# Optimization experiments

Hardware: AMD Instinct MI355X
Metric: run time of the kernel (lower is better)

The kernel has to match this reference:

```python
import jax, jax.numpy as jnp
import numpy as np

RATIO = 4   # compression ratio (group size)
H = 6       # index heads
D = 64      # index head dim = max(8, 768//6//2)
TOPK = 8    # index_topk
EPS = 1e-6  # rms_norm eps


def rms_norm(x):
    return x * jax.lax.rsqrt(jnp.mean(jnp.square(x), axis=-1, keepdims=True) + EPS)


def setup_inputs() -> dict:
    key = jax.random.key(0)
    k1, k2, k3, k4, k5 = jax.random.split(key, 5)
    B, T, E = 4, 4096, 768
    s = 0.02
    return {
        "x": jax.random.normal(k1, (B, T, E), jnp.float32),
        "wq": jax.random.normal(k2, (E, H * D), jnp.float32) * s,
        "wk": jax.random.normal(k3, (E, H * D), jnp.float32) * s,
        "wg": jax.random.normal(k4, (E, H * D), jnp.float32) * s,
        "ape": jax.random.normal(k5, (RATIO, H, D), jnp.float32) * s,
    }


def reference(x, wq, wk, wg, ape):
    B, T, E = x.shape
    G = -(-T // RATIO)          # ceil(T / ratio)
    pad = G * RATIO - T

    # --- compress keys: gated pooling over ratio-groups ---
    k = (x @ wk).reshape(B, T, H, D)
    gate = (x @ wg).reshape(B, T, H, D)
    if pad:
        k = jnp.pad(k, ((0, 0), (0, pad), (0, 0), (0, 0)))
        gate = jnp.pad(gate, ((0, 0), (0, pad), (0, 0), (0, 0)), constant_values=-jnp.inf)
    k = k.reshape(B, G, RATIO, H, D)
    gate = gate.reshape(B, G, RATIO, H, D) + ape[None, None]
    w = jax.nn.softmax(gate.astype(jnp.float32), axis=2).astype(k.dtype)
    keys = rms_norm(jnp.sum(k * w, axis=2))           # [B,G,H,D]
    group_ends = jnp.minimum(jnp.arange(RATIO - 1, G * RATIO, RATIO), T - 1)  # [G]

    # --- query-key scores ---
    q = rms_norm((x @ wq).reshape(B, T, H, D))
    scores = jnp.einsum('bthd,bghd->bhtg', q, keys) * (D ** -0.5)
    scores = jnp.mean(scores, axis=1)                 # [B,T,G]

    # --- causal mask over group ends, then top-k selection ---
    causal = group_ends[None, None, :] <= jnp.arange(T)[None, :, None]  # [1,T,G]
    scores = jnp.where(causal, scores, -jnp.inf)
    topk = min(TOPK, G)
    _, sel = jax.lax.top_k(scores, topk)              # [B,T,topk]

    # scatter selected indices into boolean mask
    bi = jnp.arange(B)[:, None, None]
    ti = jnp.arange(T)[None, :, None]
    mask = jnp.zeros((B, T, G), dtype=bool).at[bi, ti, sel].set(True)
    return (mask & causal, group_ends)
```

## Files before the change

kernel.cpp:

```cpp
#include <hip/hip_runtime.h>
#include <hip/hip_bf16.h>
#include <math.h>

#define B_    4
#define T_    4096
#define E_    768
#define H_    6
#define D_    64
#define HD_   384
#define G_    1024
#define RATIO_ 4
#define TOPK_ 8
#define MT_   (B_*T_)
#define NS_   1152

typedef __attribute__((ext_vector_type(8))) short short8;
typedef __attribute__((ext_vector_type(4))) float f32x4;
typedef __hip_bfloat16 bf16;

#define GLD16(g, l) __builtin_amdgcn_global_load_lds( \
    (const __attribute__((address_space(1))) void*)(g), \
    (__attribute__((address_space(3))) void*)(l), 16, 0, 0)

static __device__ __forceinline__ unsigned short f2bf(float f) {
  bf16 h = __float2bfloat16(f);
  return __builtin_bit_cast(unsigned short, h);
}

__global__ __launch_bounds__(256) void cvt_x_kernel(
    const float* __restrict__ in, bf16* __restrict__ out)
{
  size_t i = (size_t)blockIdx.x * 256 + threadIdx.x;
  const float4* p = reinterpret_cast<const float4*>(in) + i * 2;
  float4 v0 = p[0], v1 = p[1];
  float f[8] = {v0.x, v0.y, v0.z, v0.w, v1.x, v1.y, v1.z, v1.w};
  union { unsigned short u[8]; short8 v; } r;
#pragma unroll
  for (int k = 0; k < 8; ++k) r.u[k] = f2bf(f[k]);
  *reinterpret_cast<short8*>(out + i * 8) = r.v;
}

__global__ __launch_bounds__(256) void cvt_w_t(
    const float* __restrict__ wq, const float* __restrict__ wk,
    const float* __restrict__ wg, bf16* __restrict__ outbase)
{
  const int z = blockIdx.z;
  const float* src = z == 0 ? wq : (z == 1 ? wk : wg);
  __shared__ float t[32][33];
  int r = threadIdx.x >> 5, c = threadIdx.x & 31;
  int k0 = blockIdx.x * 32, n0 = blockIdx.y * 32;
#pragma unroll
  for (int i = 0; i < 4; ++i)
    t[r + i * 8][c] = src[(size_t)(k0 + r + i * 8) * HD_ + n0 + c];
  __syncthreads();
#pragma unroll
  for (int i = 0; i < 4; ++i) {
    int cc = n0 + r + i * 8;
    int ro = (z == 0) ? cc : 384 + ((cc >> 4) << 5) + ((z - 1) << 4) + (cc & 15);
    outbase[(size_t)ro * E_ + k0 + c] = __float2bfloat16(t[c][r + i * 8]);
  }
}

__global__ __launch_bounds__(256, 3) void gemm_qkg_mfma(
    const bf16* __restrict__ X, const bf16* __restrict__ Ws,
    const float* __restrict__ ape, bf16* __restrict__ Q,
    bf16* __restrict__ keys)
{
  __shared__ bf16 lds[3][4096];
  const int tid = threadIdx.x;
  const int lane = tid & 63, wv = tid >> 6;
  const int ll = lane & 15, lh = lane >> 4;
  const int m0 = blockIdx.x * 128, n0 = blockIdx.y * 128;
  const int srow = tid >> 2;
  const int scol = (((tid & 3) ^ ((tid >> 3) & 3)) << 3);
  const bf16* pB0 = Ws + (size_t)(n0 + srow) * E_ + scol;
  const bf16* pB1 = Ws + (size_t)(n0 + 64 + srow) * E_ + scol;
  const bf16* pA0 = X + (size_t)(m0 + wv * 32 + ll) * E_ + lh * 8;
  const bf16* pA1 = pA0 + (size_t)16 * E_;

#define STAGE(b, k0) do { \
    char* base_ = (char*)&lds[b][0] + tid * 16; \
    GLD16(pB0 + (k0), base_); \
    GLD16(pB1 + (k0), base_ + 4096); \
  } while (0)

  f32x4 acc[2][8];
#pragma unroll
  for (int m = 0; m < 2; ++m)
#pragma unroll
    for (int n = 0; n < 8; ++n) acc[m][n] = (f32x4){0.f, 0.f, 0.f, 0.f};
  const int asw = (lh ^ ((ll >> 1) & 3)) << 3;

  short8 curA0 = *reinterpret_cast<const short8*>(pA0);
  short8 curA1 = *reinterpret_cast<const short8*>(pA1);
  STAGE(0, 0);
  STAGE(1, 32);
  short8 nxtA0 = curA0, nxtA1 = curA1;

#pragma unroll
  for (int k = 0; k < 24; ++k) {
    const int k0 = k * 32;
    if (k < 23) {
      nxtA0 = *reinterpret_cast<const short8*>(pA0 + k0 + 32);
      nxtA1 = *reinterpret_cast<const short8*>(pA1 + k0 + 32);
    }
    if (k < 22) STAGE((k + 2) % 3, k0 + 64);
    if (k < 22)       asm volatile("s_waitcnt vmcnt(6)" ::: "memory");
    else if (k == 22) asm volatile("s_waitcnt vmcnt(4)" ::: "memory");
    else              asm volatile("s_waitcnt vmcnt(0)" ::: "memory");
    __builtin_amdgcn_s_barrier();
    __builtin_amdgcn_sched_barrier(0);
    const bf16* Lb = &lds[k % 3][0];
    short8 b[8];
#pragma unroll
    for (int n = 0; n < 8; ++n)
      b[n] = *reinterpret_cast<const short8*>(&Lb[(n * 16 + ll) * 32 + asw]);
    asm volatile("s_waitcnt lgkmcnt(0)" ::: "memory");
    __builtin_amdgcn_sched_barrier(0);
    __builtin_amdgcn_s_barrier();
#pragma unroll
    for (int m = 0; m < 2; ++m) {
      short8 am = (m == 0) ? curA0 : curA1;
#pragma unroll
      for (int n = 0; n < 8; ++n)
        acc[m][n] = __builtin_amdgcn_mfma_f32_16x16x32_bf16(am, b[n], acc[m][n], 0, 0, 0);
    }
    curA0 = nxtA0; curA1 = nxtA1;
  }
#undef STAGE

  if (blockIdx.y < 3) {
#pragma unroll
    for (int m = 0; m < 2; ++m)
#pragma unroll
      for (int j = 0; j < 4; ++j) {
        int row = m0 + wv * 32 + m * 16 + lh * 4 + j;
#pragma unroll
        for (int h = 0; h < 2; ++h) {
          float ss = 0.f;
#pragma unroll
          for (int n = 4 * h; n < 4 * h + 4; ++n) ss += acc[m][n][j] * acc[m][n][j];
          ss += __shfl_xor(ss, 1, 64); ss += __shfl_xor(ss, 2, 64);
          ss += __shfl_xor(ss, 4, 64); ss += __shfl_xor(ss, 8, 64);
          float scl = rsqrtf(ss * (1.0f / D_) + 1e-6f);
#pragma unroll
          for (int n = 4 * h; n < 4 * h + 4; ++n)
            Q[(size_t)row * HD_ + n0 + n * 16 + ll] =
                __float2bfloat16(acc[m][n][j] * scl);
        }
      }
  } else {
    const int hcb = (n0 - 384) >> 1;
    float apev[4][4];
#pragma unroll
    for (int p = 0; p < 4; ++p) {
      int hc = hcb + p * 16 + ll;
#pragma unroll
      for (int j = 0; j < 4; ++j) apev[p][j] = ape[j * HD_ + hc];
    }
#pragma unroll
    for (int m = 0; m < 2; ++m) {
      float pooled[4];
#pragma unroll
      for (int p = 0; p < 4; ++p) {
        float g0 = acc[m][2 * p + 1][0] + apev[p][0];
        float g1 = acc[m][2 * p + 1][1] + apev[p][1];
        float g2 = acc[m][2 * p + 1][2] + apev[p][2];
        float g3 = acc[m][2 * p + 1][3] + apev[p][3];
        float mx = fmaxf(fmaxf(g0, g1), fmaxf(g2, g3));
        float e0 = expf(g0 - mx), e1 = expf(g1 - mx);
        float e2 = expf(g2 - mx), e3 = expf(g3 - mx);
        float inv = 1.0f / (e0 + e1 + e2 + e3);
        pooled[p] = (acc[m][2 * p][0] * e0 + acc[m][2 * p][1] * e1 +
                     acc[m][2 * p][2] * e2 + acc[m][2 * p][3] * e3) * inv;
      }
      float ss = pooled[0] * pooled[0] + pooled[1] * pooled[1] +
                 pooled[2] * pooled[2] + pooled[3] * pooled[3];
      ss += __shfl_xor(ss, 1, 64); ss += __shfl_xor(ss, 2, 64);
      ss += __shfl_xor(ss, 4, 64); ss += __shfl_xor(ss, 8, 64);
      float scl = rsqrtf(ss * (1.0f / D_) + 1e-6f);
      int prow = (m0 >> 2) + wv * 8 + m * 4 + lh;
#pragma unroll
      for (int p = 0; p < 4; ++p)
        keys[(size_t)prow * HD_ + hcb + p * 16 + ll] =
            __float2bfloat16(pooled[p] * scl);
    }
  }
}

__global__ __launch_bounds__(256, 4) void gemm_score_mfma(
    const bf16* __restrict__ Qall, const bf16* __restrict__ Kall,
    float* __restrict__ Call)
{
  const int m0 = blockIdx.x * 64, n0 = blockIdx.y * 128;
  if (4 * n0 >= m0 + 64) return;
  __shared__ bf16 lds[2][4096];
  const bf16* Qb = Qall + (size_t)blockIdx.z * T_ * HD_;
  const bf16* Kb = Kall + (size_t)blockIdx.z * G_ * HD_;
  float* C = Call + (size_t)blockIdx.z * T_ * G_;
  const int tid = threadIdx.x;
  const int lane = tid & 63, wv = tid >> 6;
  const int wm = wv >> 1, wn = wv & 1;
  const int ll = lane & 15, lh = lane >> 4;
  const int srow = tid >> 2;
  const int scol = (((tid & 3) ^ ((tid >> 3) & 3)) << 3);
  const bf16* pB0 = Kb + (size_t)(n0 + srow) * HD_ + scol;
  const bf16* pB1 = Kb + (size_t)(n0 + 64 + srow) * HD_ + scol;
  const bf16* pA0 = Qb + (size_t)(m0 + wm * 32 + ll) * HD_ + lh * 8;
  const bf16* pA1 = pA0 + (size_t)16 * HD_;

#define S_STAGE(b, k0) do { \
    char* base_ = (char*)&lds[b][0] + tid * 16; \
    GLD16(pB0 + (k0), base_); \
    GLD16(pB1 + (k0), base_ + 4096); \
  } while (0)

  f32x4 acc[2][4];
#pragma unroll
  for (int m = 0; m < 2; ++m)
#pragma unroll
    for (int n = 0; n < 4; ++n) acc[m][n] = (f32x4){0.f, 0.f, 0.f, 0.f};
  const int asw = (lh ^ ((ll >> 1) & 3)) << 3;

  S_STAGE(0, 0);
  __syncthreads();
  for (int k0 = 0; k0 < HD_; k0 += 32) {
    const int cur = (k0 >> 5) & 1;
    if (k0 + 32 < HD_) S_STAGE(cur ^ 1, k0 + 32);
    short8 a[2], b[4];
    a[0] = *reinterpret_cast<const short8*>(pA0 + k0);
    a[1] = *reinterpret_cast<const short8*>(pA1 + k0);
    const bf16* Lb = &lds[cur][0];
#pragma unroll
    for (int n = 0; n < 4; ++n)
      b[n] = *reinterpret_cast<const short8*>(&Lb[(wn * 64 + n * 16 + ll) * 32 + asw]);
#pragma unroll
    for (int m = 0; m < 2; ++m)
#pragma unroll
      for (int n = 0; n < 4; ++n)
        acc[m][n] = __builtin_amdgcn_mfma_f32_16x16x32_bf16(a[m], b[n], acc[m][n], 0, 0, 0);
    __syncthreads();
  }
#undef S_STAGE
  const float scale = 0.125f / 6.0f;
#pragma unroll
  for (int m = 0; m < 2; ++m)
#pragma unroll
    for (int j = 0; j < 4; ++j) {
      int row = m0 + wm * 32 + m * 16 + lh * 4 + j;
#pragma unroll
      for (int n = 0; n < 4; ++n)
        C[(size_t)row * G_ + n0 + wn * 64 + n * 16 + ll] = acc[m][n][j] * scale;
    }
}

__global__ __launch_bounds__(256) void topk_kernel(float* __restrict__ scores,
                                                   int* __restrict__ ends)
{
  if (blockIdx.x == 0) {
    int g = threadIdx.x;
#pragma unroll
    for (int c = 0; c < 4; ++c, g += 256) {
      int e = g * RATIO_ + RATIO_ - 1;
      ends[g] = (e < T_ - 1 ? e : T_ - 1);
    }
  }
  const int r = blockIdx.x * 4 + (threadIdx.x >> 6);
  const int lane = threadIdx.x & 63;
  const int t = r & (T_ - 1);
  const int gmax = (t + 1) >> 2;
  float* row = scores + (size_t)r * G_;
  const int base = lane << 4;
  const float4* p = reinterpret_cast<const float4*>(row + base);
  float4 xv[4];
#pragma unroll
  for (int c = 0; c < 4; ++c) {
    if (base + 4 * c < gmax) xv[c] = p[c];
    else xv[c] = make_float4(-INFINITY, -INFINITY, -INFINITY, -INFINITY);
  }
  float v[16] = {xv[0].x, xv[0].y, xv[0].z, xv[0].w,
                 xv[1].x, xv[1].y, xv[1].z, xv[1].w,
                 xv[2].x, xv[2].y, xv[2].z, xv[2].w,
                 xv[3].x, xv[3].y, xv[3].z, xv[3].w};
#pragma unroll
  for (int j = 0; j < 16; ++j)
    if (base + j >= gmax) v[j] = -INFINITY;
  float lv = v[0]; int li = 0;
#pragma unroll
  for (int j = 1; j < 16; ++j)
    if (v[j] > lv) { lv = v[j]; li = j; }
  unsigned sel = 0;
  const int nsel = gmax < TOPK_ ? gmax : TOPK_;
  for (int it = 0; it < nsel; ++it) {
    float bv = lv; int bi = base + li;
#pragma unroll
    for (int off = 1; off < 64; off <<= 1) {
      float ov = __shfl_xor(bv, off, 64);
      int oi = __shfl_xor(bi, off, 64);
      if (ov > bv || (ov == bv && oi < bi)) { bv = ov; bi = oi; }
    }
    if ((bi >> 4) == lane) {
      sel |= 1u << (bi & 15);
      v[bi & 15] = -INFINITY;
      lv = v[0]; li = 0;
#pragma unroll
      for (int j = 1; j < 16; ++j)
        if (v[j] > lv) { lv = v[j]; li = j; }
    }
  }
  int4* q = reinterpret_cast<int4*>(row + base);
#pragma unroll
  for (int c = 0; c < 4; ++c)
    q[c] = make_int4((sel >> (4 * c)) & 1, (sel >> (4 * c + 1)) & 1,
                     (sel >> (4 * c + 2)) & 1, (sel >> (4 * c + 3)) & 1);
}

extern "C" void kernel_launch(void* const* d_in, const int* in_sizes, int n_in,
                              void* d_out, int out_size, void* d_ws, size_t ws_size,
                              hipStream_t stream)
{
  const float* x   = (const float*)d_in[0];
  const float* wq  = (const float*)d_in[1];
  const float* wk  = (const float*)d_in[2];
  const float* wg  = (const float*)d_in[3];
  const float* ape = (const float*)d_in[4];

  bf16* Ws   = (bf16*)d_ws;
  bf16* qb   = Ws + (size_t)NS_ * E_;
  bf16* keys = qb + (size_t)MT_ * HD_;

  bf16* xb = (bf16*)d_out;

  cvt_x_kernel<<<dim3(MT_ * E_ / 8 / 256), dim3(256), 0, stream>>>(x, xb);
  cvt_w_t<<<dim3(E_ / 32, HD_ / 32, 3), dim3(256), 0, stream>>>(wq, wk, wg, Ws);

  gemm_qkg_mfma<<<dim3(MT_ / 128, NS_ / 128), dim3(256), 0, stream>>>(
      xb, Ws, ape, qb, keys);

  gemm_score_mfma<<<dim3(T_ / 64, G_ / 128, B_), dim3(256), 0, stream>>>(
      qb, keys, (float*)d_out);

  topk_kernel<<<dim3(MT_ / 4), dim3(256), 0, stream>>>(
      (float*)d_out, (int*)d_out + (size_t)B_ * T_ * G_);
}
```

Baseline: 124.1 us.

## Fuse score GEMM with register top-k using packed sortable keys

Replaces the separate score GEMM, which wrote a full fp32 score matrix, and the following top-k pass with one single-wave kernel per 16 query rows. Each wave streams key tiles through MFMA while holding its Q fragments in registers, packs each score with its index into a monotone unsigned key, and keeps a running top-8 through an insertion network. Lane results are merged with a shuffle-based bitonic merge, then the mask rows are zeroed and the selected entries set. This removes the round trip of the score matrix through memory, but it truncates score mantissa bits (so near-ties may resolve differently) and drops LDS reuse of K across waves.

```diff
diff --git a/kernel.cpp b/kernel.cpp
--- a/kernel.cpp
+++ b/kernel.cpp
@@ -26,6 +26,8 @@
   bf16 h = __float2bfloat16(f);
   return __builtin_bit_cast(unsigned short, h);
 }
+static __device__ __forceinline__ unsigned umax_(unsigned a, unsigned b) { return a > b ? a : b; }
+static __device__ __forceinline__ unsigned umin_(unsigned a, unsigned b) { return a > b ? b : a; }
 
 __global__ __launch_bounds__(256) void cvt_x_kernel(
     const float* __restrict__ in, bf16* __restrict__ out)
@@ -188,131 +190,126 @@
   }
 }
 
-__global__ __launch_bounds__(256, 4) void gemm_score_mfma(
+__global__ __launch_bounds__(64, 1) void score_topk_fused(
     const bf16* __restrict__ Qall, const bf16* __restrict__ Kall,
-    float* __restrict__ Call)
-{
-  const int m0 = blockIdx.x * 64, n0 = blockIdx.y * 128;
-  if (4 * n0 >= m0 + 64) return;
-  __shared__ bf16 lds[2][4096];
-  const bf16* Qb = Qall + (size_t)blockIdx.z * T_ * HD_;
-  const bf16* Kb = Kall + (size_t)blockIdx.z * G_ * HD_;
-  float* C = Call + (size_t)blockIdx.z * T_ * G_;
-  const int tid = threadIdx.x;
-  const int lane = tid & 63, wv = tid >> 6;
-  const int wm = wv >> 1, wn = wv & 1;
+    int* __restrict__ mask, int* __restrict__ ends)
+{
+  const int W = blockIdx.x;
+  const int lane = threadIdx.x;
   const int ll = lane & 15, lh = lane >> 4;
-  const int srow = tid >> 2;
-  const int scol = (((tid & 3) ^ ((tid >> 3) & 3)) << 3);
-  const bf16* pB0 = Kb + (size_t)(n0 + srow) * HD_ + scol;
-  const bf16* pB1 = Kb + (size_t)(n0 + 64 + srow) * HD_ + scol;
-  const bf16* pA0 = Qb + (size_t)(m0 + wm * 32 + ll) * HD_ + lh * 8;
-  const bf16* pA1 = pA0 + (size_t)16 * HD_;
-
-#define S_STAGE(b, k0) do { \
-    char* base_ = (char*)&lds[b][0] + tid * 16; \
-    GLD16(pB0 + (k0), base_); \
-    GLD16(pB1 + (k0), base_ + 4096); \
-  } while (0)
-
-  f32x4 acc[2][4];
-#pragma unroll
-  for (int m = 0; m < 2; ++m)
-#pragma unroll
-    for (int n = 0; n < 4; ++n) acc[m][n] = (f32x4){0.f, 0.f, 0.f, 0.f};
-  const int asw = (lh ^ ((ll >> 1) & 3)) << 3;
-
-  S_STAGE(0, 0);
-  __syncthreads();
-  for (int k0 = 0; k0 < HD_; k0 += 32) {
-    const int cur = (k0 >> 5) & 1;
-    if (k0 + 32 < HD_) S_STAGE(cur ^ 1, k0 + 32);
-    short8 a[2], b[4];
-    a[0] = *reinterpret_cast<const short8*>(pA0 + k0);
-    a[1] = *reinterpret_cast<const short8*>(pA1 + k0);
-    const bf16* Lb = &lds[cur][0];
-#pragma unroll
-    for (int n = 0; n < 4; ++n)
-      b[n] = *reinterpret_cast<const short8*>(&Lb[(wn * 64 + n * 16 + ll) * 32 + asw]);
-#pragma unroll
-    for (int m = 0; m < 2; ++m)
-#pragma unroll
-      for (int n = 0; n < 4; ++n)
-        acc[m][n] = __builtin_amdgcn_mfma_f32_16x16x32_bf16(a[m], b[n], acc[m][n], 0, 0, 0);
-    __syncthreads();
-  }
-#undef S_STAGE
-  const float scale = 0.125f / 6.0f;
-#pragma unroll
-  for (int m = 0; m < 2; ++m)
-#pragma unroll
-    for (int j = 0; j < 4; ++j) {
-      int row = m0 + wm * 32 + m * 16 + lh * 4 + j;
-#pragma unroll
-      for (int n = 0; n < 4; ++n)
-        C[(size_t)row * G_ + n0 + wn * 64 + n * 16 + ll] = acc[m][n][j] * scale;
-    }
-}
-
-__global__ __launch_bounds__(256) void topk_kernel(float* __restrict__ scores,
-                                                   int* __restrict__ ends)
-{
-  if (blockIdx.x == 0) {
-    int g = threadIdx.x;
-#pragma unroll
-    for (int c = 0; c < 4; ++c, g += 256) {
-      int e = g * RATIO_ + RATIO_ - 1;
-      ends[g] = (e < T_ - 1 ? e : T_ - 1);
-    }
-  }
-  const int r = blockIdx.x * 4 + (threadIdx.x >> 6);
-  const int lane = threadIdx.x & 63;
-  const int t = r & (T_ - 1);
+  const int b = W >> 8;
+  const int t0 = (W & 255) << 4;
+
+  if (W == 0) {
+#pragma unroll
+    for (int i = 0; i < 16; ++i) {
+      int g = lane + (i << 6);
+      int e = (g << 2) + 3;
+      ends[g] = e < T_ - 1 ? e : T_ - 1;
+    }
+  }
+
+  const bf16* Qb = Qall + (size_t)b * T_ * HD_;
+  const bf16* Kb = Kall + (size_t)b * G_ * HD_;
+  const int t = t0 + ll;
   const int gmax = (t + 1) >> 2;
-  float* row = scores + (size_t)r * G_;
-  const int base = lane << 4;
-  const float4* p = reinterpret_cast<const float4*>(row + base);
-  float4 xv[4];
-#pragma unroll
-  for (int c = 0; c < 4; ++c) {
-    if (base + 4 * c < gmax) xv[c] = p[c];
-    else xv[c] = make_float4(-INFINITY, -INFINITY, -INFINITY, -INFINITY);
-  }
-  float v[16] = {xv[0].x, xv[0].y, xv[0].z, xv[0].w,
-                 xv[1].x, xv[1].y, xv[1].z, xv[1].w,
-                 xv[2].x, xv[2].y, xv[2].z, xv[2].w,
-                 xv[3].x, xv[3].y, xv[3].z, xv[3].w};
-#pragma unroll
-  for (int j = 0; j < 16; ++j)
-    if (base + j >= gmax) v[j] = -INFINITY;
-  float lv = v[0]; int li = 0;
-#pragma unroll
-  for (int j = 1; j < 16; ++j)
-    if (v[j] > lv) { lv = v[j]; li = j; }
-  unsigned sel = 0;
-  const int nsel = gmax < TOPK_ ? gmax : TOPK_;
-  for (int it = 0; it < nsel; ++it) {
-    float bv = lv; int bi = base + li;
-#pragma unroll
-    for (int off = 1; off < 64; off <<= 1) {
-      float ov = __shfl_xor(bv, off, 64);
-      int oi = __shfl_xor(bi, off, 64);
-      if (ov > bv || (ov == bv && oi < bi)) { bv = ov; bi = oi; }
-    }
-    if ((bi >> 4) == lane) {
-      sel |= 1u << (bi & 15);
-      v[bi & 15] = -INFINITY;
-      lv = v[0]; li = 0;
-#pragma unroll
-      for (int j = 1; j < 16; ++j)
-        if (v[j] > lv) { lv = v[j]; li = j; }
-    }
-  }
-  int4* q = reinterpret_cast<int4*>(row + base);
-#pragma unroll
-  for (int c = 0; c < 4; ++c)
-    q[c] = make_int4((sel >> (4 * c)) & 1, (sel >> (4 * c + 1)) & 1,
-                     (sel >> (4 * c + 2)) & 1, (sel >> (4 * c + 3)) & 1);
+  const int nmega = ((t0 >> 2) + 4 + 63) >> 6;
+
+  short8 qf[12];
+  {
+    const bf16* pQ = Qb + (size_t)t * HD_ + lh * 8;
+#pragma unroll
+    for (int k = 0; k < 12; ++k)
+      qf[k] = *reinterpret_cast<const short8*>(pQ + k * 32);
+  }
+
+  unsigned v0 = 0, v1 = 0, v2 = 0, v3 = 0, v4 = 0, v5 = 0, v6 = 0, v7 = 0;
+#define INS(x) do { unsigned k_ = (x), t_; \
+    t_ = umax_(v0, k_); k_ = umin_(v0, k_); v0 = t_; \
+    t_ = umax_(v1, k_); k_ = umin_(v1, k_); v1 = t_; \
+    t_ = umax_(v2, k_); k_ = umin_(v2, k_); v2 = t_; \
+    t_ = umax_(v3, k_); k_ = umin_(v3, k_); v3 = t_; \
+    t_ = umax_(v4, k_); k_ = umin_(v4, k_); v4 = t_; \
+    t_ = umax_(v5, k_); k_ = umin_(v5, k_); v5 = t_; \
+    t_ = umax_(v6, k_); k_ = umin_(v6, k_); v6 = t_; \
+    t_ = umax_(v7, k_); k_ = umin_(v7, k_); v7 = t_; } while (0)
+
+  for (int mg = 0; mg < nmega; ++mg) {
+    const int g0 = mg << 6;
+    const bf16* pK = Kb + (size_t)(g0 + ll) * HD_ + lh * 8;
+    short8 kf[12][4];
+#pragma unroll
+    for (int kk = 0; kk < 12; ++kk)
+#pragma unroll
+      for (int tl = 0; tl < 4; ++tl)
+        kf[kk][tl] = *reinterpret_cast<const short8*>(
+            pK + (size_t)tl * 16 * HD_ + kk * 32);
+    f32x4 acc[4];
+#pragma unroll
+    for (int tl = 0; tl < 4; ++tl) acc[tl] = (f32x4){0.f, 0.f, 0.f, 0.f};
+#pragma unroll
+    for (int kk = 0; kk < 12; ++kk)
+#pragma unroll
+      for (int tl = 0; tl < 4; ++tl)
+        acc[tl] = __builtin_amdgcn_mfma_f32_16x16x32_bf16(
+            kf[kk][tl], qf[kk], acc[tl], 0, 0, 0);
+#pragma unroll
+    for (int tl = 0; tl < 4; ++tl)
+#pragma unroll
+      for (int j = 0; j < 4; ++j) {
+        int g = g0 + tl * 16 + lh * 4 + j;
+        float x = acc[tl][j] + 512.0f;
+        unsigned key = (g < gmax)
+            ? ((__builtin_bit_cast(unsigned, x) & 0xFFFFFC00u) |
+               (unsigned)(1023 - g))
+            : 0u;
+        INS(key);
+      }
+  }
+#undef INS
+
+#define CEx(a, bb) { unsigned h_ = umax_(a, bb), l_ = umin_(a, bb); a = h_; bb = l_; }
+#pragma unroll
+  for (int st = 0; st < 2; ++st) {
+    const int off = 16 << st;
+    unsigned p0 = (unsigned)__shfl_xor((int)v0, off, 64);
+    unsigned p1 = (unsigned)__shfl_xor((int)v1, off, 64);
+    unsigned p2 = (unsigned)__shfl_xor((int)v2, off, 64);
+    unsigned p3 = (unsigned)__shfl_xor((int)v3, off, 64);
+    unsigned p4 = (unsigned)__shfl_xor((int)v4, off, 64);
+    unsigned p5 = (unsigned)__shfl_xor((int)v5, off, 64);
+    unsigned p6 = (unsigned)__shfl_xor((int)v6, off, 64);
+    unsigned p7 = (unsigned)__shfl_xor((int)v7, off, 64);
+    unsigned w0 = umax_(v0, p7), w1 = umax_(v1, p6);
+    unsigned w2 = umax_(v2, p5), w3 = umax_(v3, p4);
+    unsigned w4 = umax_(v4, p3), w5 = umax_(v5, p2);
+    unsigned w6 = umax_(v6, p1), w7 = umax_(v7, p0);
+    CEx(w0, w4); CEx(w1, w5); CEx(w2, w6); CEx(w3, w7);
+    CEx(w0, w2); CEx(w1, w3); CEx(w4, w6); CEx(w5, w7);
+    CEx(w0, w1); CEx(w2, w3); CEx(w4, w5); CEx(w6, w7);
+    v0 = w0; v1 = w1; v2 = w2; v3 = w3; v4 = w4; v5 = w5; v6 = w6; v7 = w7;
+  }
+#undef CEx
+
+  int* mbase = mask + ((size_t)b * T_ + t0) * G_;
+  const int4 z = make_int4(0, 0, 0, 0);
+#pragma unroll
+  for (int r = 0; r < 16; ++r)
+#pragma unroll
+    for (int c = 0; c < 4; ++c)
+      *reinterpret_cast<int4*>(mbase + (size_t)r * G_ + (c << 8) + (lane << 2)) = z;
+  asm volatile("s_waitcnt vmcnt(0)" ::: "memory");
+  if (lh == 0) {
+    int* rb = mbase + (size_t)ll * G_;
+    if (v0) rb[1023 - (v0 & 1023)] = 1;
+    if (v1) rb[1023 - (v1 & 1023)] = 1;
+    if (v2) rb[1023 - (v2 & 1023)] = 1;
+    if (v3) rb[1023 - (v3 & 1023)] = 1;
+    if (v4) rb[1023 - (v4 & 1023)] = 1;
+    if (v5) rb[1023 - (v5 & 1023)] = 1;
+    if (v6) rb[1023 - (v6 & 1023)] = 1;
+    if (v7) rb[1023 - (v7 & 1023)] = 1;
+  }
 }
 
 extern "C" void kernel_launch(void* const* d_in, const int* in_sizes, int n_in,
@@ -337,9 +334,6 @@
   gemm_qkg_mfma<<<dim3(MT_ / 128, NS_ / 128), dim3(256), 0, stream>>>(
       xb, Ws, ape, qb, keys);
 
-  gemm_score_mfma<<<dim3(T_ / 64, G_ / 128, B_), dim3(256), 0, stream>>>(
-      qb, keys, (float*)d_out);
-
-  topk_kernel<<<dim3(MT_ / 4), dim3(256), 0, stream>>>(
-      (float*)d_out, (int*)d_out + (size_t)B_ * T_ * G_);
-}
+  score_topk_fused<<<dim3(MT_ / 16), dim3(64), 0, stream>>>(
+      qb, keys, (int*)d_out, (int*)d_out + (size_t)B_ * T_ * G_);
+}
```

New measurement: 175.8 us. 1.42x slower.
